# Kernel tuning notes

Measured on AMD Instinct MI355X. Metric: run time of the kernel, lower is better.

## Reference

```python
import jax, jax.numpy as jnp
import numpy as np

B, PP, LP, H = 128, 1024, 128, 256  # graphs, protein atoms/graph, ligand atoms/graph, hidden
NP, NL = B * PP, B * LP


def setup_inputs() -> dict:
    key = jax.random.key(0)
    ks = jax.random.split(key, 16)
    s = 0.02
    return {
        "protein_pos": 10.0 * jax.random.normal(ks[0], (NP, 3), jnp.float32),
        "ligand_pos": 10.0 * jax.random.normal(ks[1], (NL, 3), jnp.float32),
        "protein_element": jax.random.randint(ks[2], (NP,), 0, 128),
        "protein_aa": jax.random.randint(ks[3], (NP,), 0, 32),
        "protein_is_backbone": jax.random.randint(ks[4], (NP,), 0, 2),
        "ligand_type": jax.random.randint(ks[5], (NL,), 0, 16),
        "protein_batch": jnp.repeat(jnp.arange(B), PP),  # block-contiguous segments
        "ligand_batch": jnp.repeat(jnp.arange(B), LP),
        "E_elem": s * jax.random.normal(ks[6], (128, H), jnp.float32),
        "E_aa": s * jax.random.normal(ks[7], (32, H), jnp.float32),
        "E_bb": s * jax.random.normal(ks[8], (2, H), jnp.float32),
        "E_lig": s * jax.random.normal(ks[9], (16, H), jnp.float32),
        "Wd1": s * jax.random.normal(ks[10], (H, H), jnp.float32),
        "bd1": jnp.zeros((H,), jnp.float32),
        "Wd2": s * jax.random.normal(ks[11], (H, H), jnp.float32),
        "bd2": jnp.zeros((H,), jnp.float32),
        "Wa1": s * jax.random.normal(ks[12], (2 * H + 2, H), jnp.float32),
        "ba1": jnp.zeros((H,), jnp.float32),
        "Wa2": s * jax.random.normal(ks[13], (H, 1), jnp.float32),
        "ba2": jnp.zeros((1,), jnp.float32),
    }


def _pool_by_batch(x, batch, bsz):
    # mean-pool rows of x into bsz segments (index_add_ + bincount in torch)
    summed = jax.ops.segment_sum(x, batch, num_segments=bsz)
    counts = jax.ops.segment_sum(jnp.ones((x.shape[0],), x.dtype), batch, num_segments=bsz)
    return summed / jnp.maximum(counts, 1.0)[:, None]


def reference(protein_pos, ligand_pos, protein_element, protein_aa, protein_is_backbone,
              ligand_type, protein_batch, ligand_batch,
              E_elem, E_aa, E_bb, E_lig, Wd1, bd1, Wd2, bd2, Wa1, ba1, Wa2, ba2):
    # protein / ligand node embeddings
    h_protein = E_elem[protein_element] + E_aa[protein_aa] + E_bb[protein_is_backbone]
    h_ligand = E_lig[ligand_type]

    # compose_context: protein first, then ligand (mask_ligand = [0]*NP + [1]*NL)
    h_ctx = jnp.concatenate([h_protein, h_ligand], axis=0)

    # stub denoiser: pointwise 2-layer SiLU MLP producing out['h']
    h_out = jax.nn.silu(h_ctx @ Wd1 + bd1) @ Wd2 + bd2
    protein_h = h_out[:protein_pos.shape[0]]
    ligand_h = h_out[protein_pos.shape[0]:]

    pooled_protein = _pool_by_batch(protein_h, protein_batch, B)  # [B, H]
    pooled_ligand = _pool_by_batch(ligand_h, ligand_batch, B)     # [B, H]

    # contact features: per-graph cdist(lig, prot), min over protein atoms,
    # then mean & min over ligand atoms. Uniform block layout -> dense reshape.
    prot = protein_pos.reshape(B, PP, 3)
    lig = ligand_pos.reshape(B, LP, 3)
    d2 = jnp.sum((lig[:, :, None, :] - prot[:, None, :, :]) ** 2, axis=-1)  # [B, LP, PP]
    dist = jnp.sqrt(d2)
    min_lp = dist.min(axis=2)                                    # [B, LP]
    contact = jnp.stack([min_lp.mean(axis=1), min_lp.min(axis=1)], axis=-1)  # [B, 2]

    graph_feat = jnp.concatenate([pooled_protein, pooled_ligand, contact], axis=-1)  # [B, 2H+2]
    affinity = (jax.nn.silu(graph_feat @ Wa1 + ba1) @ Wa2 + ba2).squeeze(-1)  # [B]
    return affinity
```

## Files before the change

kernel.cpp:

```cpp
#include <hip/hip_runtime.h>
#include <hip/hip_bf16.h>

typedef _Float16 f16;
typedef _Float16 h4 __attribute__((ext_vector_type(4)));
typedef float f32x4 __attribute__((ext_vector_type(4)));

#define B_   128
#define PP_  1024
#define LP_  128
#define H_   256
#define NP_  131072
#define NL_  16384


__global__ void __launch_bounds__(256) prep_k(
    const float* __restrict__ W1,
    const float* __restrict__ Ee, const float* __restrict__ Ea,
    const float* __restrict__ Eb, const float* __restrict__ El,
    const float* __restrict__ bd1, const float* __restrict__ W2,
    const float* __restrict__ Wa1, const float* __restrict__ ba1,
    const float* __restrict__ bd2,
    f16* __restrict__ tbl, float* __restrict__ wc, float* __restrict__ cvec,
    float* __restrict__ ysum)
{
  __shared__ float src[256];
  const int bid = blockIdx.x, tid = threadIdx.x;
  if (bid < 256) ysum[bid * 256 + tid] = 0.f;

  if (bid < 178) {
    const float* s;
    float badd = 0.f;
    if (bid < 128)      s = Ee + bid * 256;
    else if (bid < 160) s = Ea + (bid - 128) * 256;
    else if (bid < 162) { s = Eb + (bid - 160) * 256; badd = bd1[tid]; }
    else                { s = El + (bid - 162) * 256; badd = bd1[tid]; }
    src[tid] = s[tid];
    __syncthreads();
    float a0 = 0.f, a1 = 0.f, a2 = 0.f, a3 = 0.f;
#pragma unroll 4
    for (int k = 0; k < 256; k += 4) {
      a0 += src[k]     * W1[(k)     * 256 + tid];
      a1 += src[k + 1] * W1[(k + 1) * 256 + tid];
      a2 += src[k + 2] * W1[(k + 2) * 256 + tid];
      a3 += src[k + 3] * W1[(k + 3) * 256 + tid];
    }
    tbl[bid * 256 + tid] = (f16)(((a0 + a1) + (a2 + a3)) + badd);
  } else if (bid < 690) {
    const int r = bid - 178;
    const int half = r >> 8, rr = r & 255;
    src[tid] = W2[rr * 256 + tid];
    __syncthreads();
    const float* W = Wa1 + half * 256 * 256 + tid;
    float a0 = 0.f, a1 = 0.f, a2 = 0.f, a3 = 0.f;
#pragma unroll 4
    for (int n = 0; n < 256; n += 4) {
      a0 += src[n]     * W[(n)     * 256];
      a1 += src[n + 1] * W[(n + 1) * 256];
      a2 += src[n + 2] * W[(n + 2) * 256];
      a3 += src[n + 3] * W[(n + 3) * 256];
    }
    const float scale = half ? (1.f / (float)LP_) : (1.f / (float)PP_);
    wc[half * 65536 + rr * 256 + tid] = ((a0 + a1) + (a2 + a3)) * scale;
  } else {
    float a = ba1[tid];
#pragma unroll 8
    for (int n = 0; n < 256; ++n)
      a += bd2[n] * (Wa1[n * 256 + tid] + Wa1[(256 + n) * 256 + tid]);
    cvec[tid] = a;
  }
}

__global__ void __launch_bounds__(256, 4) gpool_k(
    const int* __restrict__ pel, const int* __restrict__ paa,
    const int* __restrict__ pbb, const int* __restrict__ ltyp,
    const f16* __restrict__ tbl, float* __restrict__ ysum)
{
  const int tid = threadIdx.x, wave = tid >> 6, lane = tid & 63;
  const int batch = blockIdx.x / 18, g = blockIdx.x % 18;
  const int c0 = lane * 4;
  f32x4 acc = (f32x4){0.f, 0.f, 0.f, 0.f};

  if (g < 16) {
    const int base = batch * PP_ + g * 64 + wave * 16;
#pragma unroll 4
    for (int r = 0; r < 16; ++r) {
      const int idx = base + r;
      h4 va = *(const h4*)(tbl + pel[idx] * 256 + c0);
      h4 vb = *(const h4*)(tbl + 32768 + paa[idx] * 256 + c0);
      h4 vc = *(const h4*)(tbl + 40960 + pbb[idx] * 256 + c0);
#pragma unroll
      for (int i = 0; i < 4; ++i) {
        float pre = (float)va[i] + (float)vb[i] + (float)vc[i];
        acc[i] += pre * __builtin_amdgcn_rcpf(1.f + __expf(-pre));
      }
    }
  } else {
    const int base = batch * LP_ + (g - 16) * 64 + wave * 16;
#pragma unroll 4
    for (int r = 0; r < 16; ++r) {
      const int idx = base + r;
      h4 v = *(const h4*)(tbl + 41472 + ltyp[idx] * 256 + c0);
#pragma unroll
      for (int i = 0; i < 4; ++i) {
        float pre = (float)v[i];
        acc[i] += pre * __builtin_amdgcn_rcpf(1.f + __expf(-pre));
      }
    }
  }

  __shared__ f32x4 red[3][64];
  if (wave) red[wave - 1][lane] = acc;
  __syncthreads();
  if (wave == 0) {
    f32x4 a1 = red[0][lane], a2 = red[1][lane], a3 = red[2][lane];
    float* pool = ysum + (g < 16 ? 0 : 32768) + batch * 256 + c0;
#pragma unroll
    for (int i = 0; i < 4; ++i)
      atomicAdd(pool + i, ((acc[i] + a1[i]) + (a2[i] + a3[i])));
  }
}

__global__ void __launch_bounds__(512) head_k(
    const float* __restrict__ ppos, const float* __restrict__ lpos,
    const float* __restrict__ ysum, const float* __restrict__ wc,
    const float* __restrict__ cvec, const float* __restrict__ Wa1,
    const float* __restrict__ Wa2, const float* __restrict__ ba2,
    float* __restrict__ out)
{
  __shared__ float px[4 * 264], py[4 * 264], pz[4 * 264];
  __shared__ float ysc[512];
  __shared__ float part[512];
  __shared__ float lmin[128];
  __shared__ float cls[2];
  __shared__ float red[4];
  const int b = blockIdx.x, tid = threadIdx.x;

#pragma unroll
  for (int r = 0; r < 2; ++r) {
    const int i = r * 512 + tid;
    const int d = (i >> 8) * 264 + (i & 255);
    const float* p = ppos + ((size_t)b * PP_ + i) * 3;
    px[d] = p[0]; py[d] = p[1]; pz[d] = p[2];
  }
  ysc[tid] = (tid < 256) ? ysum[b * 256 + tid]
                         : ysum[32768 + b * 256 + (tid - 256)];
  __syncthreads();

  {
    const int lig = tid >> 2, prt = tid & 3;
    const float* lp = lpos + ((size_t)b * LP_ + lig) * 3;
    const float lx = lp[0], ly = lp[1], lz = lp[2];
    const float4* X4 = (const float4*)(px + prt * 264);
    const float4* Y4 = (const float4*)(py + prt * 264);
    const float4* Z4 = (const float4*)(pz + prt * 264);
    float m = 3.4e38f;
#pragma unroll 4
    for (int i = 0; i < 64; ++i) {
      float4 X = X4[i], Y = Y4[i], Z = Z4[i];
      float dx, dy, dz, d2;
      dx = lx - X.x; dy = ly - Y.x; dz = lz - Z.x;
      d2 = dx * dx + dy * dy + dz * dz; m = fminf(m, d2);
      dx = lx - X.y; dy = ly - Y.y; dz = lz - Z.y;
      d2 = dx * dx + dy * dy + dz * dz; m = fminf(m, d2);
      dx = lx - X.z; dy = ly - Y.z; dz = lz - Z.z;
      d2 = dx * dx + dy * dy + dz * dz; m = fminf(m, d2);
      dx = lx - X.w; dy = ly - Y.w; dz = lz - Z.w;
      d2 = dx * dx + dy * dy + dz * dz; m = fminf(m, d2);
    }
    m = fminf(m, __shfl_xor(m, 1));
    m = fminf(m, __shfl_xor(m, 2));
    if (prt == 0) lmin[lig] = sqrtf(m);
  }
  __syncthreads();
  if (tid < 64) {
    const float a0 = lmin[tid], a1 = lmin[tid + 64];
    float sm = a0 + a1, mn = fminf(a0, a1);
#pragma unroll
    for (int off = 32; off; off >>= 1) {
      sm += __shfl_down(sm, off);
      mn = fminf(mn, __shfl_down(mn, off));
    }
    if (tid == 0) { cls[0] = sm * (1.f / (float)LP_); cls[1] = mn; }
  }

  {
    const int gg = tid >> 8, j = tid & 255;
    const float* W = wc + gg * 65536 + j;
    const float* ys = ysc + gg * 256;
    float a[8];
#pragma unroll
    for (int u = 0; u < 8; ++u) a[u] = 0.f;
#pragma unroll 2
    for (int k = 0; k < 256; k += 8) {
#pragma unroll
      for (int u = 0; u < 8; ++u)
        a[u] += ys[k + u] * W[(k + u) * 256];
    }
    part[tid] = ((a[0] + a[1]) + (a[2] + a[3])) + ((a[4] + a[5]) + (a[6] + a[7]));
  }
  __syncthreads();

  if (tid < 256) {
    float pre = part[tid] + part[256 + tid] + cvec[tid]
              + cls[0] * Wa1[512 * 256 + tid] + cls[1] * Wa1[513 * 256 + tid];
    float si = pre * __builtin_amdgcn_rcpf(1.f + __expf(-pre));
    float p = si * Wa2[tid];
#pragma unroll
    for (int off = 32; off; off >>= 1) p += __shfl_down(p, off);
    if ((tid & 63) == 0) red[tid >> 6] = p;
  }
  __syncthreads();
  if (tid == 0) out[b] = (red[0] + red[1]) + (red[2] + red[3]) + ba2[0];
}

extern "C" void kernel_launch(void* const* d_in, const int* in_sizes, int n_in,
                              void* d_out, int out_size, void* d_ws, size_t ws_size,
                              hipStream_t stream)
{
  const float* protein_pos = (const float*)d_in[0];
  const float* ligand_pos  = (const float*)d_in[1];
  const int*   pel  = (const int*)d_in[2];
  const int*   paa  = (const int*)d_in[3];
  const int*   pbb  = (const int*)d_in[4];
  const int*   ltyp = (const int*)d_in[5];
  const float* Ee  = (const float*)d_in[8];
  const float* Ea  = (const float*)d_in[9];
  const float* Eb  = (const float*)d_in[10];
  const float* El  = (const float*)d_in[11];
  const float* Wd1 = (const float*)d_in[12];
  const float* bd1 = (const float*)d_in[13];
  const float* Wd2 = (const float*)d_in[14];
  const float* bd2 = (const float*)d_in[15];
  const float* Wa1 = (const float*)d_in[16];
  const float* ba1 = (const float*)d_in[17];
  const float* Wa2 = (const float*)d_in[18];
  const float* ba2 = (const float*)d_in[19];
  float* out = (float*)d_out;

  char* ws = (char*)d_ws;
  f16*   tbl  = (f16*)(ws);
  float* ysum = (float*)(ws + 98304);
  float* wc   = (float*)(ws + 360448);
  float* cvec = (float*)(ws + 884736);

  prep_k<<<691, 256, 0, stream>>>(Wd1, Ee, Ea, Eb, El, bd1, Wd2, Wa1, ba1, bd2,
                                  tbl, wc, cvec, ysum);
  gpool_k<<<B_ * 18, 256, 0, stream>>>(pel, paa, pbb, ltyp, tbl, ysum);
  head_k<<<B_, 512, 0, stream>>>(protein_pos, ligand_pos, ysum, wc, cvec,
                                 Wa1, Wa2, ba2, out);
}
```

Baseline: 137.5 us.

## Rebalance kernels: move contact distance and wc precompute into the pooling launch

Splits the prep kernel so only the embedding-table projection and ysum zeroing run first. The Wa1-folding (wc, cvec) work and the ligand-protein min-distance computation move into a merged middle kernel that also does the gather/SiLU pooling. The distance work is split into two blocks per graph, each covering half the protein atoms. The head kernel then reads precomputed partial minima from a new workspace buffer. The goal is to spread the serial distance scan over more blocks and overlap independent work inside one large launch, at the cost of a heterogeneous kernel and an extra global round-trip for the minima.

Result: faster. 131.2 us (median of 2 runs) (-4.5%).

```diff
diff --git a/kernel.cpp b/kernel.cpp
--- a/kernel.cpp
+++ b/kernel.cpp
@@ -13,121 +13,162 @@
 #define NL_  16384
 
 
-__global__ void __launch_bounds__(256) prep_k(
+__global__ void __launch_bounds__(256) tbl_k(
     const float* __restrict__ W1,
     const float* __restrict__ Ee, const float* __restrict__ Ea,
     const float* __restrict__ Eb, const float* __restrict__ El,
-    const float* __restrict__ bd1, const float* __restrict__ W2,
-    const float* __restrict__ Wa1, const float* __restrict__ ba1,
-    const float* __restrict__ bd2,
-    f16* __restrict__ tbl, float* __restrict__ wc, float* __restrict__ cvec,
-    float* __restrict__ ysum)
+    const float* __restrict__ bd1,
+    f16* __restrict__ tbl, float* __restrict__ ysum)
 {
   __shared__ float src[256];
   const int bid = blockIdx.x, tid = threadIdx.x;
-  if (bid < 256) ysum[bid * 256 + tid] = 0.f;
-
-  if (bid < 178) {
-    const float* s;
-    float badd = 0.f;
-    if (bid < 128)      s = Ee + bid * 256;
-    else if (bid < 160) s = Ea + (bid - 128) * 256;
-    else if (bid < 162) { s = Eb + (bid - 160) * 256; badd = bd1[tid]; }
-    else                { s = El + (bid - 162) * 256; badd = bd1[tid]; }
-    src[tid] = s[tid];
+  ysum[bid * 256 + tid] = 0.f;
+  if (bid >= 178) return;
+
+  const float* s;
+  float badd = 0.f;
+  if (bid < 128)      s = Ee + bid * 256;
+  else if (bid < 160) s = Ea + (bid - 128) * 256;
+  else if (bid < 162) { s = Eb + (bid - 160) * 256; badd = bd1[tid]; }
+  else                { s = El + (bid - 162) * 256; badd = bd1[tid]; }
+  src[tid] = s[tid];
+  __syncthreads();
+  float a0 = 0.f, a1 = 0.f, a2 = 0.f, a3 = 0.f;
+#pragma unroll 4
+  for (int k = 0; k < 256; k += 4) {
+    a0 += src[k]     * W1[(k)     * 256 + tid];
+    a1 += src[k + 1] * W1[(k + 1) * 256 + tid];
+    a2 += src[k + 2] * W1[(k + 2) * 256 + tid];
+    a3 += src[k + 3] * W1[(k + 3) * 256 + tid];
+  }
+  tbl[bid * 256 + tid] = (f16)(((a0 + a1) + (a2 + a3)) + badd);
+}
+
+__global__ void __launch_bounds__(256, 4) mid_k(
+    const float* __restrict__ W2, const float* __restrict__ Wa1,
+    const float* __restrict__ ba1, const float* __restrict__ bd2,
+    const float* __restrict__ ppos, const float* __restrict__ lpos,
+    const int* __restrict__ pel, const int* __restrict__ paa,
+    const int* __restrict__ pbb, const int* __restrict__ ltyp,
+    const f16* __restrict__ tbl,
+    float* __restrict__ wc, float* __restrict__ cvec,
+    float* __restrict__ gmin, float* __restrict__ ysum)
+{
+  __shared__ __align__(16) float sm[1536];
+  const int bid = blockIdx.x, tid = threadIdx.x;
+
+  if (bid < 512) {
+    const int half = bid >> 8, rr = bid & 255;
+    sm[tid] = W2[rr * 256 + tid];
     __syncthreads();
+    const float* W = Wa1 + half * 65536 + tid;
     float a0 = 0.f, a1 = 0.f, a2 = 0.f, a3 = 0.f;
 #pragma unroll 4
-    for (int k = 0; k < 256; k += 4) {
-      a0 += src[k]     * W1[(k)     * 256 + tid];
-      a1 += src[k + 1] * W1[(k + 1) * 256 + tid];
-      a2 += src[k + 2] * W1[(k + 2) * 256 + tid];
-      a3 += src[k + 3] * W1[(k + 3) * 256 + tid];
-    }
-    tbl[bid * 256 + tid] = (f16)(((a0 + a1) + (a2 + a3)) + badd);
-  } else if (bid < 690) {
-    const int r = bid - 178;
-    const int half = r >> 8, rr = r & 255;
-    src[tid] = W2[rr * 256 + tid];
-    __syncthreads();
-    const float* W = Wa1 + half * 256 * 256 + tid;
-    float a0 = 0.f, a1 = 0.f, a2 = 0.f, a3 = 0.f;
-#pragma unroll 4
     for (int n = 0; n < 256; n += 4) {
-      a0 += src[n]     * W[(n)     * 256];
-      a1 += src[n + 1] * W[(n + 1) * 256];
-      a2 += src[n + 2] * W[(n + 2) * 256];
-      a3 += src[n + 3] * W[(n + 3) * 256];
+      a0 += sm[n]     * W[(n)     * 256];
+      a1 += sm[n + 1] * W[(n + 1) * 256];
+      a2 += sm[n + 2] * W[(n + 2) * 256];
+      a3 += sm[n + 3] * W[(n + 3) * 256];
     }
     const float scale = half ? (1.f / (float)LP_) : (1.f / (float)PP_);
     wc[half * 65536 + rr * 256 + tid] = ((a0 + a1) + (a2 + a3)) * scale;
-  } else {
+
+  } else if (bid == 512) {
     float a = ba1[tid];
 #pragma unroll 8
     for (int n = 0; n < 256; ++n)
       a += bd2[n] * (Wa1[n * 256 + tid] + Wa1[(256 + n) * 256 + tid]);
     cvec[tid] = a;
-  }
-}
-
-__global__ void __launch_bounds__(256, 4) gpool_k(
-    const int* __restrict__ pel, const int* __restrict__ paa,
-    const int* __restrict__ pbb, const int* __restrict__ ltyp,
-    const f16* __restrict__ tbl, float* __restrict__ ysum)
-{
-  const int tid = threadIdx.x, wave = tid >> 6, lane = tid & 63;
-  const int batch = blockIdx.x / 18, g = blockIdx.x % 18;
-  const int c0 = lane * 4;
-  f32x4 acc = (f32x4){0.f, 0.f, 0.f, 0.f};
-
-  if (g < 16) {
-    const int base = batch * PP_ + g * 64 + wave * 16;
-#pragma unroll 4
-    for (int r = 0; r < 16; ++r) {
-      const int idx = base + r;
-      h4 va = *(const h4*)(tbl + pel[idx] * 256 + c0);
-      h4 vb = *(const h4*)(tbl + 32768 + paa[idx] * 256 + c0);
-      h4 vc = *(const h4*)(tbl + 40960 + pbb[idx] * 256 + c0);
-#pragma unroll
-      for (int i = 0; i < 4; ++i) {
-        float pre = (float)va[i] + (float)vb[i] + (float)vc[i];
-        acc[i] += pre * __builtin_amdgcn_rcpf(1.f + __expf(-pre));
+
+  } else if (bid < 769) {
+    const int cb = bid - 513, b = cb >> 1, half = cb & 1;
+    float* px = sm;
+    float* py = sm + 512;
+    float* pz = sm + 1024;
+#pragma unroll
+    for (int r = 0; r < 2; ++r) {
+      const int i = r * 256 + tid;
+      const float* p = ppos + ((size_t)b * PP_ + half * 512 + i) * 3;
+      px[i] = p[0]; py[i] = p[1]; pz[i] = p[2];
+    }
+    __syncthreads();
+    const int lig = tid >> 1, part = tid & 1;
+    const float* lp = lpos + ((size_t)b * LP_ + lig) * 3;
+    const float lx = lp[0], ly = lp[1], lz = lp[2];
+    const float4* X4 = (const float4*)(px + part * 256);
+    const float4* Y4 = (const float4*)(py + part * 256);
+    const float4* Z4 = (const float4*)(pz + part * 256);
+    float m = 3.4e38f;
+#pragma unroll 4
+    for (int i = 0; i < 64; ++i) {
+      float4 X = X4[i], Y = Y4[i], Z = Z4[i];
+      float dx, dy, dz, d2;
+      dx = lx - X.x; dy = ly - Y.x; dz = lz - Z.x;
+      d2 = dx * dx + dy * dy + dz * dz; m = fminf(m, d2);
+      dx = lx - X.y; dy = ly - Y.y; dz = lz - Z.y;
+      d2 = dx * dx + dy * dy + dz * dz; m = fminf(m, d2);
+      dx = lx - X.z; dy = ly - Y.z; dz = lz - Z.z;
+      d2 = dx * dx + dy * dy + dz * dz; m = fminf(m, d2);
+      dx = lx - X.w; dy = ly - Y.w; dz = lz - Z.w;
+      d2 = dx * dx + dy * dy + dz * dz; m = fminf(m, d2);
+    }
+    m = fminf(m, __shfl_xor(m, 1));
+    if (!part) gmin[cb * 128 + lig] = m;
+
+  } else {
+    const int idx = bid - 769;
+    const int batch = idx / 18, g = idx % 18;
+    const int wave = tid >> 6, lane = tid & 63;
+    const int c0 = lane * 4;
+    f32x4 acc = (f32x4){0.f, 0.f, 0.f, 0.f};
+
+    if (g < 16) {
+      const int base = batch * PP_ + g * 64 + wave * 16;
+#pragma unroll 4
+      for (int r = 0; r < 16; ++r) {
+        const int i = base + r;
+        h4 va = *(const h4*)(tbl + pel[i] * 256 + c0);
+        h4 vb = *(const h4*)(tbl + 32768 + paa[i] * 256 + c0);
+        h4 vc = *(const h4*)(tbl + 40960 + pbb[i] * 256 + c0);
+#pragma unroll
+        for (int k = 0; k < 4; ++k) {
+          float pre = (float)va[k] + (float)vb[k] + (float)vc[k];
+          acc[k] += pre * __builtin_amdgcn_rcpf(1.f + __expf(-pre));
+        }
       }
-    }
-  } else {
-    const int base = batch * LP_ + (g - 16) * 64 + wave * 16;
-#pragma unroll 4
-    for (int r = 0; r < 16; ++r) {
-      const int idx = base + r;
-      h4 v = *(const h4*)(tbl + 41472 + ltyp[idx] * 256 + c0);
-#pragma unroll
-      for (int i = 0; i < 4; ++i) {
-        float pre = (float)v[i];
-        acc[i] += pre * __builtin_amdgcn_rcpf(1.f + __expf(-pre));
+    } else {
+      const int base = batch * LP_ + (g - 16) * 64 + wave * 16;
+#pragma unroll 4
+      for (int r = 0; r < 16; ++r) {
+        const int i = base + r;
+        h4 v = *(const h4*)(tbl + 41472 + ltyp[i] * 256 + c0);
+#pragma unroll
+        for (int k = 0; k < 4; ++k) {
+          float pre = (float)v[k];
+          acc[k] += pre * __builtin_amdgcn_rcpf(1.f + __expf(-pre));
+        }
       }
     }
-  }
-
-  __shared__ f32x4 red[3][64];
-  if (wave) red[wave - 1][lane] = acc;
-  __syncthreads();
-  if (wave == 0) {
-    f32x4 a1 = red[0][lane], a2 = red[1][lane], a3 = red[2][lane];
-    float* pool = ysum + (g < 16 ? 0 : 32768) + batch * 256 + c0;
-#pragma unroll
-    for (int i = 0; i < 4; ++i)
-      atomicAdd(pool + i, ((acc[i] + a1[i]) + (a2[i] + a3[i])));
+
+    f32x4* red = (f32x4*)sm;
+    if (wave) red[(wave - 1) * 64 + lane] = acc;
+    __syncthreads();
+    if (wave == 0) {
+      f32x4 a1 = red[lane], a2 = red[64 + lane], a3 = red[128 + lane];
+      float* pool = ysum + (g < 16 ? 0 : 32768) + batch * 256 + c0;
+#pragma unroll
+      for (int k = 0; k < 4; ++k)
+        atomicAdd(pool + k, ((acc[k] + a1[k]) + (a2[k] + a3[k])));
+    }
   }
 }
 
 __global__ void __launch_bounds__(512) head_k(
-    const float* __restrict__ ppos, const float* __restrict__ lpos,
     const float* __restrict__ ysum, const float* __restrict__ wc,
     const float* __restrict__ cvec, const float* __restrict__ Wa1,
     const float* __restrict__ Wa2, const float* __restrict__ ba2,
-    float* __restrict__ out)
-{
-  __shared__ float px[4 * 264], py[4 * 264], pz[4 * 264];
+    const float* __restrict__ gmin, float* __restrict__ out)
+{
   __shared__ float ysc[512];
   __shared__ float part[512];
   __shared__ float lmin[128];
@@ -135,43 +176,14 @@
   __shared__ float red[4];
   const int b = blockIdx.x, tid = threadIdx.x;
 
-#pragma unroll
-  for (int r = 0; r < 2; ++r) {
-    const int i = r * 512 + tid;
-    const int d = (i >> 8) * 264 + (i & 255);
-    const float* p = ppos + ((size_t)b * PP_ + i) * 3;
-    px[d] = p[0]; py[d] = p[1]; pz[d] = p[2];
-  }
   ysc[tid] = (tid < 256) ? ysum[b * 256 + tid]
                          : ysum[32768 + b * 256 + (tid - 256)];
-  __syncthreads();
-
-  {
-    const int lig = tid >> 2, prt = tid & 3;
-    const float* lp = lpos + ((size_t)b * LP_ + lig) * 3;
-    const float lx = lp[0], ly = lp[1], lz = lp[2];
-    const float4* X4 = (const float4*)(px + prt * 264);
-    const float4* Y4 = (const float4*)(py + prt * 264);
-    const float4* Z4 = (const float4*)(pz + prt * 264);
-    float m = 3.4e38f;
-#pragma unroll 4
-    for (int i = 0; i < 64; ++i) {
-      float4 X = X4[i], Y = Y4[i], Z = Z4[i];
-      float dx, dy, dz, d2;
-      dx = lx - X.x; dy = ly - Y.x; dz = lz - Z.x;
-      d2 = dx * dx + dy * dy + dz * dz; m = fminf(m, d2);
-      dx = lx - X.y; dy = ly - Y.y; dz = lz - Z.y;
-      d2 = dx * dx + dy * dy + dz * dz; m = fminf(m, d2);
-      dx = lx - X.z; dy = ly - Y.z; dz = lz - Z.z;
-      d2 = dx * dx + dy * dy + dz * dz; m = fminf(m, d2);
-      dx = lx - X.w; dy = ly - Y.w; dz = lz - Z.w;
-      d2 = dx * dx + dy * dy + dz * dz; m = fminf(m, d2);
-    }
-    m = fminf(m, __shfl_xor(m, 1));
-    m = fminf(m, __shfl_xor(m, 2));
-    if (prt == 0) lmin[lig] = sqrtf(m);
-  }
-  __syncthreads();
+  if (tid < 128) {
+    const float m = fminf(gmin[(b * 2) * 128 + tid], gmin[(b * 2 + 1) * 128 + tid]);
+    lmin[tid] = sqrtf(m);
+  }
+  __syncthreads();
+
   if (tid < 64) {
     const float a0 = lmin[tid], a1 = lmin[tid + 64];
     float sm = a0 + a1, mn = fminf(a0, a1);
@@ -242,10 +254,10 @@
   float* ysum = (float*)(ws + 98304);
   float* wc   = (float*)(ws + 360448);
   float* cvec = (float*)(ws + 884736);
-
-  prep_k<<<691, 256, 0, stream>>>(Wd1, Ee, Ea, Eb, El, bd1, Wd2, Wa1, ba1, bd2,
-                                  tbl, wc, cvec, ysum);
-  gpool_k<<<B_ * 18, 256, 0, stream>>>(pel, paa, pbb, ltyp, tbl, ysum);
-  head_k<<<B_, 512, 0, stream>>>(protein_pos, ligand_pos, ysum, wc, cvec,
-                                 Wa1, Wa2, ba2, out);
-}
+  float* gmin = (float*)(ws + 885760);
+
+  tbl_k<<<256, 256, 0, stream>>>(Wd1, Ee, Ea, Eb, El, bd1, tbl, ysum);
+  mid_k<<<3073, 256, 0, stream>>>(Wd2, Wa1, ba1, bd2, protein_pos, ligand_pos,
+                                  pel, paa, pbb, ltyp, tbl, wc, cvec, gmin, ysum);
+  head_k<<<B_, 512, 0, stream>>>(ysum, wc, cvec, Wa1, Wa2, ba2, gmin, out);
+}
```
